# Performance work log

Hardware: AMD Instinct MI355X
Metric: run time of the kernel (lower is better)

Reference implementation:

```python
import jax, jax.numpy as jnp
import numpy as np

IN, OUT, HID = 256, 256, 512
BATCH, T = 16, 4096


def setup_inputs() -> dict:
    key = jax.random.key(0)
    ks = jax.random.split(key, 10)
    # nu/theta init as in the original module (r_min=0, r_max=1)
    u1 = jax.random.uniform(ks[0], (HID,))
    nu = -0.5 * jnp.log(u1)  # uniform in (0,1) -> nu > 0
    nu_log = jnp.log(nu)
    theta = (jnp.pi / 10.0) * jax.random.uniform(ks[1], (HID,))
    theta_log = jnp.log(theta)
    # glorot-uniform style scales
    sB = float(np.sqrt(6.0 / (HID + IN)))
    sC = float(np.sqrt(6.0 / (OUT + HID)))
    sD = float(np.sqrt(6.0 / (OUT + IN)))
    B_re = jax.random.uniform(ks[2], (HID, IN), minval=-sB, maxval=sB)
    B_im = jax.random.uniform(ks[3], (HID, IN), minval=-sB, maxval=sB)
    C_re = jax.random.uniform(ks[4], (OUT, HID), minval=-sC, maxval=sC)
    C_im = jax.random.uniform(ks[5], (OUT, HID), minval=-sC, maxval=sC)
    D = jax.random.uniform(ks[6], (OUT, IN), minval=-sD, maxval=sD)
    bh_re = jnp.zeros((HID,), jnp.float32)
    bh_im = jnp.zeros((HID,), jnp.float32)
    bias_output = jnp.zeros((OUT,), jnp.float32)
    X = jax.random.normal(ks[7], (BATCH, T, IN), dtype=jnp.float32)
    return {
        "X": X, "nu_log": nu_log, "theta_log": theta_log,
        "B_re": B_re, "B_im": B_im, "C_re": C_re, "C_im": C_im,
        "D": D, "bh_re": bh_re, "bh_im": bh_im, "bias_output": bias_output,
    }


def reference(X, nu_log, theta_log, B_re, B_im, C_re, C_im, D, bh_re, bh_im, bias_output):
    # lambda = exp(-exp(nu_log) + i*exp(theta_log));  |lambda| = exp(-exp(nu_log))
    mag = jnp.exp(-jnp.exp(nu_log))                       # [H], real
    lam = mag * jnp.exp(1j * jnp.exp(theta_log))          # [H], complex64
    gamma = jnp.sqrt(1.0 - mag * mag)                     # [H], real
    B = B_re + 1j * B_im                                  # [H, I]
    C = C_re + 1j * C_im                                  # [O, H]
    bias_h = bh_re + 1j * bh_im                           # [H]
    # input drive precomputed for all timesteps: gamma * (B @ x_t) + bias_hidden
    Bu = jnp.einsum("bti,hi->bth", X.astype(jnp.complex64), B)  # [B,T,H]
    drive = gamma.astype(jnp.complex64) * Bu + bias_h           # [B,T,H]

    def step(h, d_t):  # h: [B,H] complex, d_t: [B,H] complex
        h = lam * h + d_t
        return h, h

    h0 = jnp.zeros((X.shape[0], lam.shape[0]), jnp.complex64)
    _, H = jax.lax.scan(step, h0, jnp.swapaxes(drive, 0, 1))  # H: [T,B,H]
    H = jnp.swapaxes(H, 0, 1)                                 # [B,T,H]
    Y = (jnp.real(jnp.einsum("bth,oh->bto", H, C))
         + jnp.einsum("bti,oi->bto", X, D)
         + bias_output)
    return Y
```

## Files before the change

kernel.cpp:

```cpp
#include <hip/hip_runtime.h>
#include <hip/hip_bf16.h>


#define TT     4096
#define BATCHN 16
#define MM     (BATCHN * TT)
#define LCH    64
#define NCH    (TT / LCH)

typedef unsigned short u16;
typedef short bf16x8 __attribute__((ext_vector_type(8)));
typedef float f32x4 __attribute__((ext_vector_type(4)));

__device__ __forceinline__ u16 f2bf(float f) {
  union { __hip_bfloat16 b; u16 u; } cv;
  cv.b = __float2bfloat16(f);
  return cv.u;
}
__device__ __forceinline__ float bf2f(u16 u) {
  union { u16 u; __hip_bfloat16 b; } cv;
  cv.u = u;
  return __bfloat162float(cv.b);
}

__global__ void k_params(const float* __restrict__ nu_log,
                         const float* __restrict__ theta_log,
                         float* __restrict__ P) {
  int h = threadIdx.x;
  if (h >= 512) return;
  double nu  = exp((double)nu_log[h]);
  double th  = exp((double)theta_log[h]);
  double mag = exp(-nu);
  double g   = sqrt(fmax(0.0, 1.0 - mag * mag));
  double magL = exp(-(double)LCH * nu);
  double aL   = (double)LCH * th;
  P[h]        = (float)(mag * cos(th));
  P[512 + h]  = (float)(mag * sin(th));
  P[1024 + h] = (float)g;
  P[1536 + h] = (float)(magL * cos(aL));
  P[2048 + h] = (float)(magL * sin(aL));
}

__global__ void k_prep_w(const float* __restrict__ Bre, const float* __restrict__ Bim,
                         const float* __restrict__ Cre, const float* __restrict__ Cim,
                         const float* __restrict__ D, u16* __restrict__ Bcat,
                         u16* __restrict__ Ccat) {
  const int NB = 1024 * 256;
  const int NC = 256 * 1280;
  for (int idx = blockIdx.x * blockDim.x + threadIdx.x; idx < NB + NC;
       idx += gridDim.x * blockDim.x) {
    if (idx < NB) {
      int row = idx >> 8, col = idx & 255;
      float v = (row < 512) ? Bre[row * 256 + col] : Bim[(row - 512) * 256 + col];
      Bcat[idx] = f2bf(v);
    } else {
      int j = idx - NB;
      int o = j / 1280, k = j % 1280;
      float v;
      if (k < 1024) {
        int q = k >> 9, kk = k & 511;
        int h = q * 256 + (kk & 255);
        v = (kk < 256) ? Cre[o * 512 + h] : -Cim[o * 512 + h];
      } else {
        v = D[o * 256 + (k - 1024)];
      }
      Ccat[j] = f2bf(v);
    }
  }
}

__global__ __launch_bounds__(256) void k_prep_x(const float* __restrict__ X,
                                                u16* __restrict__ Xb) {
  int idx = blockIdx.x * 256 + threadIdx.x;
  const float4* s = (const float4*)X + (size_t)idx * 2;
  float4 a = s[0], b = s[1];
  u16 o[8] = {f2bf(a.x), f2bf(a.y), f2bf(a.z), f2bf(a.w),
              f2bf(b.x), f2bf(b.y), f2bf(b.z), f2bf(b.w)};
  *(int4*)(Xb + (size_t)idx * 8) = *(const int4*)o;
}

__global__ __launch_bounds__(256) void k_gemm1(
    const u16* __restrict__ Xb, const u16* __restrict__ Bcat,
    const float* __restrict__ P, const float* __restrict__ bhr,
    const float* __restrict__ bhi, u16* __restrict__ Hbuf) {
  __shared__ __align__(16) char smem[2 * 128 * 64 * 2];
  char* sA = smem;
  char* sB = smem + 128 * 64 * 2;
  const int tid = threadIdx.x;
  const int lane = tid & 63;
  const int wid = tid >> 6;
  const int wr = wid >> 1, wc = wid & 1;
  const int mb = blockIdx.x * 128;
  const int nb = blockIdx.y * 128;

  f32x4 acc[4][4];
#pragma unroll
  for (int r = 0; r < 4; ++r)
#pragma unroll
    for (int c = 0; c < 4; ++c) acc[r][c] = (f32x4)0.f;

  for (int kt = 0; kt < 4; ++kt) {
    const int k0 = kt * 64;
    __syncthreads();
#pragma unroll
    for (int i = 0; i < 4; ++i) {
      int s = i * 256 + tid;
      int row = s >> 3, slot = s & 7;
      int4 va = *(const int4*)(Xb + (size_t)(mb + row) * 256 + k0 + slot * 8);
      int4 vb = *(const int4*)(Bcat + (size_t)(nb + row) * 256 + k0 + slot * 8);
      int soff = row * 128 + ((slot ^ (row & 7)) << 4);
      *(int4*)(sA + soff) = va;
      *(int4*)(sB + soff) = vb;
    }
    __syncthreads();
#pragma unroll
    for (int kk = 0; kk < 2; ++kk) {
      bf16x8 af[4], bfr[4];
#pragma unroll
      for (int r = 0; r < 4; ++r) {
        int row = wr * 64 + r * 16 + (lane & 15);
        int slot = (kk * 4 + (lane >> 4)) ^ (row & 7);
        af[r] = *(const bf16x8*)(sA + row * 128 + slot * 16);
      }
#pragma unroll
      for (int c = 0; c < 4; ++c) {
        int row = wc * 64 + c * 16 + (lane & 15);
        int slot = (kk * 4 + (lane >> 4)) ^ (row & 7);
        bfr[c] = *(const bf16x8*)(sB + row * 128 + slot * 16);
      }
#pragma unroll
      for (int r = 0; r < 4; ++r)
#pragma unroll
        for (int c = 0; c < 4; ++c)
          acc[r][c] = __builtin_amdgcn_mfma_f32_16x16x32_bf16(af[r], bfr[c],
                                                              acc[r][c], 0, 0, 0);
    }
  }
  const int rbase = (lane >> 4) * 4;
  const int cbase = lane & 15;
#pragma unroll
  for (int r = 0; r < 4; ++r)
#pragma unroll
    for (int c = 0; c < 4; ++c) {
      int col = nb + wc * 64 + c * 16 + cbase;
      int h = col & 511;
      float g = P[1024 + h];
      float bias = (col < 512) ? bhr[h] : bhi[h];
#pragma unroll
      for (int q = 0; q < 4; ++q) {
        int row = mb + wr * 64 + r * 16 + rbase + q;
        Hbuf[(size_t)row * 1024 + col] = f2bf(fmaf(acc[r][c][q], g, bias));
      }
    }
}

__global__ __launch_bounds__(512) void k_scanF(
    const float* __restrict__ P, const u16* __restrict__ Hbuf,
    float* __restrict__ finr, float* __restrict__ fini) {
  const int h = threadIdx.x;
  const int b = blockIdx.x, c = blockIdx.y;
  const float lr = P[h], li = P[512 + h];
  float hr = 0.f, hi = 0.f;
  size_t base = ((size_t)b * TT + (size_t)c * LCH) * 1024 + h;
#pragma unroll 8
  for (int j = 0; j < LCH; ++j) {
    float dr = bf2f(Hbuf[base]);
    float di = bf2f(Hbuf[base + 512]);
    float nr = fmaf(lr, hr, fmaf(-li, hi, dr));
    float ni = fmaf(lr, hi, fmaf(li, hr, di));
    hr = nr; hi = ni;
    base += 1024;
  }
  size_t f = ((size_t)b * NCH + c) * 512 + h;
  finr[f] = hr; fini[f] = hi;
}

__global__ __launch_bounds__(512) void k_carry(
    const float* __restrict__ P, const float* __restrict__ finr,
    const float* __restrict__ fini, float* __restrict__ carr,
    float* __restrict__ cari) {
  const int h = threadIdx.x;
  const int b = blockIdx.x;
  const float Lr = P[1536 + h], Li = P[2048 + h];
  float cr = 0.f, ci = 0.f;
  for (int c = 0; c < NCH; ++c) {
    size_t idx = ((size_t)b * NCH + c) * 512 + h;
    carr[idx] = cr; cari[idx] = ci;
    float fr = finr[idx], fi = fini[idx];
    float nr = fmaf(Lr, cr, fmaf(-Li, ci, fr));
    float ni = fmaf(Lr, ci, fmaf(Li, cr, fi));
    cr = nr; ci = ni;
  }
}

__global__ __launch_bounds__(256) void k_fused2(
    const float* __restrict__ P, const u16* __restrict__ Hbuf,
    const u16* __restrict__ Xb, const u16* __restrict__ Ccat,
    const float* __restrict__ carr, const float* __restrict__ cari,
    const float* __restrict__ bo, float* __restrict__ Y) {
  __shared__ __align__(16) char Hs[64 * 1024];
  const int tid = threadIdx.x;
  const int lane = tid & 63;
  const int w = tid >> 6;
  const int c = blockIdx.x;
  const int b = blockIdx.y;
  const int row0 = b * TT + c * LCH;

  f32x4 acc[4][4];
#pragma unroll
  for (int m = 0; m < 4; ++m)
#pragma unroll
    for (int n = 0; n < 4; ++n) acc[m][n] = (f32x4)0.f;

#pragma unroll
  for (int q = 0; q < 2; ++q) {
    const int h = q * 256 + tid;
    const float lr = P[h], li = P[512 + h];
    size_t cidx = ((size_t)b * NCH + c) * 512 + h;
    float hr = carr[cidx], hi = cari[cidx];
    size_t base = (size_t)row0 * 1024 + h;
    __syncthreads();
#pragma unroll 8
    for (int j = 0; j < LCH; ++j) {
      float dr = bf2f(Hbuf[base]);
      float di = bf2f(Hbuf[base + 512]);
      float nr = fmaf(lr, hr, fmaf(-li, hi, dr));
      float ni = fmaf(lr, hi, fmaf(li, hr, di));
      hr = nr; hi = ni;
      int sre = ((tid >> 3) ^ (j & 7)) * 16 + (tid & 7) * 2;
      int sim = (((256 + tid) >> 3) ^ (j & 7)) * 16 + (tid & 7) * 2;
      *(u16*)(Hs + j * 1024 + sre) = f2bf(nr);
      *(u16*)(Hs + j * 1024 + sim) = f2bf(ni);
      base += 1024;
    }
    __syncthreads();
#pragma unroll 4
    for (int ks = 0; ks < 16; ++ks) {
      bf16x8 af[4], bfr[4];
#pragma unroll
      for (int m = 0; m < 4; ++m) {
        int row = m * 16 + (lane & 15);
        int slot = (ks * 4 + (lane >> 4)) ^ (row & 7);
        af[m] = *(const bf16x8*)(Hs + row * 1024 + slot * 16);
      }
#pragma unroll
      for (int n = 0; n < 4; ++n) {
        int col = w * 64 + n * 16 + (lane & 15);
        bfr[n] = *(const bf16x8*)(Ccat + (size_t)col * 1280 + q * 512 +
                                  ks * 32 + (lane >> 4) * 8);
      }
#pragma unroll
      for (int m = 0; m < 4; ++m)
#pragma unroll
        for (int n = 0; n < 4; ++n)
          acc[m][n] = __builtin_amdgcn_mfma_f32_16x16x32_bf16(af[m], bfr[n],
                                                              acc[m][n], 0, 0, 0);
    }
  }

  __syncthreads();
#pragma unroll
  for (int i = 0; i < 8; ++i) {
    int p = i * 256 + tid;
    int row = p >> 5, slot = p & 31;
    int4 v = *(const int4*)(Xb + (size_t)(row0 + row) * 256 +
                            ((slot ^ (row & 7)) * 8));
    *(int4*)(Hs + row * 512 + slot * 16) = v;
  }
  __syncthreads();
#pragma unroll 2
  for (int ks = 0; ks < 8; ++ks) {
    bf16x8 af[4], bfr[4];
#pragma unroll
    for (int m = 0; m < 4; ++m) {
      int row = m * 16 + (lane & 15);
      int slot = (ks * 4 + (lane >> 4)) ^ (row & 7);
      af[m] = *(const bf16x8*)(Hs + row * 512 + slot * 16);
    }
#pragma unroll
    for (int n = 0; n < 4; ++n) {
      int col = w * 64 + n * 16 + (lane & 15);
      bfr[n] = *(const bf16x8*)(Ccat + (size_t)col * 1280 + 1024 +
                                ks * 32 + (lane >> 4) * 8);
    }
#pragma unroll
    for (int m = 0; m < 4; ++m)
#pragma unroll
      for (int n = 0; n < 4; ++n)
        acc[m][n] = __builtin_amdgcn_mfma_f32_16x16x32_bf16(af[m], bfr[n],
                                                            acc[m][n], 0, 0, 0);
  }

  const int rb = (lane >> 4) * 4;
  const int cb = lane & 15;
#pragma unroll
  for (int m = 0; m < 4; ++m)
#pragma unroll
    for (int n = 0; n < 4; ++n) {
      int col = w * 64 + n * 16 + cb;
      float bias = bo[col];
#pragma unroll
      for (int qq = 0; qq < 4; ++qq) {
        int row = row0 + m * 16 + rb + qq;
        Y[(size_t)row * 256 + col] = acc[m][n][qq] + bias;
      }
    }
}

extern "C" void kernel_launch(void* const* d_in, const int* in_sizes, int n_in,
                              void* d_out, int out_size, void* d_ws, size_t ws_size,
                              hipStream_t stream) {
  const float* X        = (const float*)d_in[0];
  const float* nu_log   = (const float*)d_in[1];
  const float* theta_lg = (const float*)d_in[2];
  const float* Bre      = (const float*)d_in[3];
  const float* Bim      = (const float*)d_in[4];
  const float* Cre      = (const float*)d_in[5];
  const float* Cim      = (const float*)d_in[6];
  const float* D        = (const float*)d_in[7];
  const float* bhr      = (const float*)d_in[8];
  const float* bhi      = (const float*)d_in[9];
  const float* bo       = (const float*)d_in[10];
  float* Y = (float*)d_out;
  char* ws = (char*)d_ws;

  size_t off = 0;
  float* P = (float*)(ws + off);            off += 2560 * 4;
  off = (off + 255) & ~(size_t)255;
  u16* Hbuf = (u16*)(ws + off);             off += (size_t)MM * 1024 * 2;
  u16* Xb   = (u16*)(ws + off);             off += (size_t)MM * 256 * 2;
  u16* Bcat = (u16*)(ws + off);             off += 1024 * 256 * 2;
  u16* Ccat = (u16*)(ws + off);             off += 256 * 1280 * 2;
  float* finr = (float*)(ws + off);         off += (size_t)BATCHN * NCH * 512 * 4;
  float* fini = (float*)(ws + off);         off += (size_t)BATCHN * NCH * 512 * 4;
  float* carr = (float*)(ws + off);         off += (size_t)BATCHN * NCH * 512 * 4;
  float* cari = (float*)(ws + off);         off += (size_t)BATCHN * NCH * 512 * 4;
  if (ws_size < off) return;

  k_params<<<1, 512, 0, stream>>>(nu_log, theta_lg, P);
  k_prep_w<<<512, 256, 0, stream>>>(Bre, Bim, Cre, Cim, D, Bcat, Ccat);
  k_prep_x<<<MM * 256 / (256 * 8), 256, 0, stream>>>(X, Xb);
  k_gemm1<<<dim3(MM / 128, 8), 256, 0, stream>>>(Xb, Bcat, P, bhr, bhi, Hbuf);
  k_scanF<<<dim3(BATCHN, NCH), 512, 0, stream>>>(P, Hbuf, finr, fini);
  k_carry<<<BATCHN, 512, 0, stream>>>(P, finr, fini, carr, cari);
  k_fused2<<<dim3(NCH, BATCHN), 256, 0, stream>>>(P, Hbuf, Xb, Ccat, carr, cari,
                                                  bo, Y);
}
```

Measured before the change: 324.2 us.

## Interleave re/im in hidden buffer and halve scan chunk length

Stores the hidden drive with real and imaginary parts interleaved, so each scan step reads one 32-bit word instead of two separate 16-bit loads. It also writes packed pairs into shared memory and reorders the C weight columns to match the interleaved layout. The chunk length drops from 64 to 32, which doubles the number of blocks in the scan and fused kernels and shortens the serial recurrence per block, but also doubles the carry-propagation length and halves the MFMA tile rows per block.

New measurement: 434.8 us. 1.34x slower.

```diff
diff --git a/kernel.cpp b/kernel.cpp
--- a/kernel.cpp
+++ b/kernel.cpp
@@ -5,10 +5,11 @@
 #define TT     4096
 #define BATCHN 16
 #define MM     (BATCHN * TT)
-#define LCH    64
+#define LCH    32
 #define NCH    (TT / LCH)
 
 typedef unsigned short u16;
+typedef unsigned int u32;
 typedef short bf16x8 __attribute__((ext_vector_type(8)));
 typedef float f32x4 __attribute__((ext_vector_type(4)));
 
@@ -58,9 +59,8 @@
       int o = j / 1280, k = j % 1280;
       float v;
       if (k < 1024) {
-        int q = k >> 9, kk = k & 511;
-        int h = q * 256 + (kk & 255);
-        v = (kk < 256) ? Cre[o * 512 + h] : -Cim[o * 512 + h];
+        int ch = k >> 1;
+        v = (k & 1) ? -Cim[o * 512 + ch] : Cre[o * 512 + ch];
       } else {
         v = D[o * 256 + (k - 1024)];
       }
@@ -146,10 +146,11 @@
       int h = col & 511;
       float g = P[1024 + h];
       float bias = (col < 512) ? bhr[h] : bhi[h];
+      int icol = (col < 512) ? (2 * col) : (2 * (col - 512) + 1);
 #pragma unroll
       for (int q = 0; q < 4; ++q) {
         int row = mb + wr * 64 + r * 16 + rbase + q;
-        Hbuf[(size_t)row * 1024 + col] = f2bf(fmaf(acc[r][c][q], g, bias));
+        Hbuf[(size_t)row * 1024 + icol] = f2bf(fmaf(acc[r][c][q], g, bias));
       }
     }
 }
@@ -161,15 +162,17 @@
   const int b = blockIdx.x, c = blockIdx.y;
   const float lr = P[h], li = P[512 + h];
   float hr = 0.f, hi = 0.f;
-  size_t base = ((size_t)b * TT + (size_t)c * LCH) * 1024 + h;
+  const u32* H32 = (const u32*)Hbuf;
+  size_t base = ((size_t)b * TT + (size_t)c * LCH) * 512 + h;
 #pragma unroll 8
   for (int j = 0; j < LCH; ++j) {
-    float dr = bf2f(Hbuf[base]);
-    float di = bf2f(Hbuf[base + 512]);
+    u32 pk = H32[base];
+    float dr = bf2f((u16)(pk & 0xffff));
+    float di = bf2f((u16)(pk >> 16));
     float nr = fmaf(lr, hr, fmaf(-li, hi, dr));
     float ni = fmaf(lr, hi, fmaf(li, hr, di));
     hr = nr; hi = ni;
-    base += 1024;
+    base += 512;
   }
   size_t f = ((size_t)b * NCH + c) * 512 + h;
   finr[f] = hr; fini[f] = hi;
@@ -198,7 +201,7 @@
     const u16* __restrict__ Xb, const u16* __restrict__ Ccat,
     const float* __restrict__ carr, const float* __restrict__ cari,
     const float* __restrict__ bo, float* __restrict__ Y) {
-  __shared__ __align__(16) char Hs[64 * 1024];
+  __shared__ __align__(16) char Hs[32 * 1024];
   const int tid = threadIdx.x;
   const int lane = tid & 63;
   const int w = tid >> 6;
@@ -206,39 +209,40 @@
   const int b = blockIdx.y;
   const int row0 = b * TT + c * LCH;
 
-  f32x4 acc[4][4];
-#pragma unroll
-  for (int m = 0; m < 4; ++m)
+  f32x4 acc[2][4];
+#pragma unroll
+  for (int m = 0; m < 2; ++m)
 #pragma unroll
     for (int n = 0; n < 4; ++n) acc[m][n] = (f32x4)0.f;
 
+  const u32* H32 = (const u32*)Hbuf;
+
 #pragma unroll
   for (int q = 0; q < 2; ++q) {
-    const int h = q * 256 + tid;
-    const float lr = P[h], li = P[512 + h];
-    size_t cidx = ((size_t)b * NCH + c) * 512 + h;
+    const int ch = q * 256 + tid;
+    const float lr = P[ch], li = P[512 + ch];
+    size_t cidx = ((size_t)b * NCH + c) * 512 + ch;
     float hr = carr[cidx], hi = cari[cidx];
-    size_t base = (size_t)row0 * 1024 + h;
+    size_t base = (size_t)row0 * 512 + ch;
     __syncthreads();
 #pragma unroll 8
     for (int j = 0; j < LCH; ++j) {
-      float dr = bf2f(Hbuf[base]);
-      float di = bf2f(Hbuf[base + 512]);
+      u32 pk = H32[base];
+      float dr = bf2f((u16)(pk & 0xffff));
+      float di = bf2f((u16)(pk >> 16));
       float nr = fmaf(lr, hr, fmaf(-li, hi, dr));
       float ni = fmaf(lr, hi, fmaf(li, hr, di));
       hr = nr; hi = ni;
-      int sre = ((tid >> 3) ^ (j & 7)) * 16 + (tid & 7) * 2;
-      int sim = (((256 + tid) >> 3) ^ (j & 7)) * 16 + (tid & 7) * 2;
-      *(u16*)(Hs + j * 1024 + sre) = f2bf(nr);
-      *(u16*)(Hs + j * 1024 + sim) = f2bf(ni);
-      base += 1024;
+      int soff = ((tid >> 2) ^ (j & 7)) * 16 + (tid & 3) * 4;
+      *(u32*)(Hs + j * 1024 + soff) = (u32)f2bf(nr) | ((u32)f2bf(ni) << 16);
+      base += 512;
     }
     __syncthreads();
 #pragma unroll 4
     for (int ks = 0; ks < 16; ++ks) {
-      bf16x8 af[4], bfr[4];
-#pragma unroll
-      for (int m = 0; m < 4; ++m) {
+      bf16x8 af[2], bfr[4];
+#pragma unroll
+      for (int m = 0; m < 2; ++m) {
         int row = m * 16 + (lane & 15);
         int slot = (ks * 4 + (lane >> 4)) ^ (row & 7);
         af[m] = *(const bf16x8*)(Hs + row * 1024 + slot * 16);
@@ -250,7 +254,7 @@
                                   ks * 32 + (lane >> 4) * 8);
       }
 #pragma unroll
-      for (int m = 0; m < 4; ++m)
+      for (int m = 0; m < 2; ++m)
 #pragma unroll
         for (int n = 0; n < 4; ++n)
           acc[m][n] = __builtin_amdgcn_mfma_f32_16x16x32_bf16(af[m], bfr[n],
@@ -260,7 +264,7 @@
 
   __syncthreads();
 #pragma unroll
-  for (int i = 0; i < 8; ++i) {
+  for (int i = 0; i < 4; ++i) {
     int p = i * 256 + tid;
     int row = p >> 5, slot = p & 31;
     int4 v = *(const int4*)(Xb + (size_t)(row0 + row) * 256 +
@@ -270,9 +274,9 @@
   __syncthreads();
 #pragma unroll 2
   for (int ks = 0; ks < 8; ++ks) {
-    bf16x8 af[4], bfr[4];
-#pragma unroll
-    for (int m = 0; m < 4; ++m) {
+    bf16x8 af[2], bfr[4];
+#pragma unroll
+    for (int m = 0; m < 2; ++m) {
       int row = m * 16 + (lane & 15);
       int slot = (ks * 4 + (lane >> 4)) ^ (row & 7);
       af[m] = *(const bf16x8*)(Hs + row * 512 + slot * 16);
@@ -284,7 +288,7 @@
                                 ks * 32 + (lane >> 4) * 8);
     }
 #pragma unroll
-    for (int m = 0; m < 4; ++m)
+    for (int m = 0; m < 2; ++m)
 #pragma unroll
       for (int n = 0; n < 4; ++n)
         acc[m][n] = __builtin_amdgcn_mfma_f32_16x16x32_bf16(af[m], bfr[n],
@@ -294,7 +298,7 @@
   const int rb = (lane >> 4) * 4;
   const int cb = lane & 15;
 #pragma unroll
-  for (int m = 0; m < 4; ++m)
+  for (int m = 0; m < 2; ++m)
 #pragma unroll
     for (int n = 0; n < 4; ++n) {
       int col = w * 64 + n * 16 + cb;
```
